# Optimization experiments

Measured on AMD Instinct MI355X. Metric: run time of the kernel, lower is better.

Reference implementation:

```python
import jax, jax.numpy as jnp
import numpy as np

B, L_SEQ, D, P, N_LAYERS, V = 2, 4096, 128, 64, 2, 32000
EPS_LN = 1e-5
EPS_Z = 1e-8


def _layernorm(x, g, b):
    mu = jnp.mean(x, axis=-1, keepdims=True)
    var = jnp.mean(jnp.square(x - mu), axis=-1, keepdims=True)
    return (x - mu) * jax.lax.rsqrt(var + EPS_LN) * g + b


def setup_inputs() -> dict:
    key = jax.random.key(0)
    ks = jax.random.split(key, 16)
    tokens = jax.random.randint(ks[0], (B, L_SEQ), 0, V)
    s = 0.02
    embed = jax.random.normal(ks[1], (V, D), jnp.float32) * s
    pos_emb = jax.random.normal(ks[2], (L_SEQ, D), jnp.float32) * s
    Wq = jax.random.normal(ks[3], (N_LAYERS, D, D), jnp.float32) * s
    Wk = jax.random.normal(ks[4], (N_LAYERS, D, D), jnp.float32) * s
    Wv = jax.random.normal(ks[5], (N_LAYERS, D, D), jnp.float32) * s
    # orthonormal random projection per layer (QR, like torch.linalg.qr reduced)
    rng = np.random.default_rng(0)
    proj_np = np.stack([np.linalg.qr(rng.standard_normal((D, P)))[0] for _ in range(N_LAYERS)])
    proj = jnp.asarray(proj_np, jnp.float32)
    ln_g = jnp.ones((N_LAYERS, D), jnp.float32)
    ln_b = jnp.zeros((N_LAYERS, D), jnp.float32)
    W1 = jax.random.normal(ks[6], (N_LAYERS, D, 4 * D), jnp.float32) * s
    b1 = jnp.zeros((N_LAYERS, 4 * D), jnp.float32)
    W2 = jax.random.normal(ks[7], (N_LAYERS, 4 * D, D), jnp.float32) * s
    b2 = jnp.zeros((N_LAYERS, D), jnp.float32)
    Wout = jax.random.normal(ks[8], (D, V), jnp.float32) * s
    return {"tokens": tokens, "embed": embed, "pos_emb": pos_emb, "Wq": Wq, "Wk": Wk,
            "Wv": Wv, "proj": proj, "ln_g": ln_g, "ln_b": ln_b, "W1": W1, "b1": b1,
            "W2": W2, "b2": b2, "Wout": Wout}


def reference(tokens, embed, pos_emb, Wq, Wk, Wv, proj, ln_g, ln_b, W1, b1, W2, b2, Wout):
    # h: [B, L, D]
    h = embed[tokens] + pos_emb[None, :, :]
    for i in range(N_LAYERS):
        residual = h
        # linear (FAVOR-style) attention, single head
        q = h @ Wq[i]
        k = h @ Wk[i]
        v = h @ Wv[i]
        q_prime = jax.nn.elu(q @ proj[i]) + 1.0  # [B, L, P]
        k_prime = jax.nn.elu(k @ proj[i]) + 1.0
        kv = jnp.einsum('blp,bld->bpd', k_prime, v)      # [B, P, D]
        num = jnp.einsum('blp,bpd->bld', q_prime, kv)     # [B, L, D]
        z = 1.0 / (jnp.sum(q_prime, axis=-1, keepdims=True) + EPS_Z)
        attn = num * z
        # LayerNorm then FFN (dropout = identity, eval mode)
        a = _layernorm(attn, ln_g[i], ln_b[i])
        f = jax.nn.gelu(a @ W1[i] + b1[i], approximate=False) @ W2[i] + b2[i]
        h = residual + f
    logits = h @ Wout  # [B, L, V]
    return logits
```

## Files before the change

kernel.cpp:

```cpp
#include <hip/hip_runtime.h>
#include <hip/hip_bf16.h>

#define BATCH 2
#define LSEQ 4096
#define M (BATCH*LSEQ)
#define D 128
#define P 64
#define NL 2
#define VOCAB 32000
#define DFF 512

typedef __attribute__((ext_vector_type(8))) short bf16x8_t;
typedef __attribute__((ext_vector_type(4))) float f32x4_t;

__device__ inline unsigned short f2bf(float f) {
    unsigned int u = __float_as_uint(f);
    unsigned int r = (u + 0x7fffu + ((u >> 16) & 1u)) >> 16;
    return (unsigned short)r;
}
__device__ inline float bf2f(unsigned short u) {
    return __uint_as_float(((unsigned int)u) << 16);
}

__global__ __launch_bounds__(256) void k_prep_all(const int* __restrict__ tokens,
                                                  const float* __restrict__ embed,
                                                  const float* __restrict__ pos,
                                                  float* __restrict__ h,
                                                  unsigned short* __restrict__ hb,
                                                  const float* __restrict__ Wout,
                                                  unsigned short* __restrict__ WT,
                                                  const float* __restrict__ Wq,
                                                  const float* __restrict__ Wk,
                                                  const float* __restrict__ Wv,
                                                  const float* __restrict__ proj,
                                                  unsigned short* __restrict__ bqkv,
                                                  const float* __restrict__ W1,
                                                  unsigned short* __restrict__ W1T,
                                                  const float* __restrict__ W2,
                                                  unsigned short* __restrict__ W2T) {
    __shared__ float tile[32][33];
    int b = blockIdx.x;
    int tid = threadIdx.x;
    if (b < 1024) {
        int gid = b * 256 + tid;
        int row = gid >> 5;
        int d4  = gid & 31;
        int l = row & (LSEQ - 1);
        int tok = tokens[row];
        float4 a = ((const float4*)(embed + (size_t)tok * D))[d4];
        float4 p4 = ((const float4*)(pos + (size_t)l * D))[d4];
        a.x += p4.x; a.y += p4.y; a.z += p4.z; a.w += p4.w;
        ((float4*)(h + (size_t)row * D))[d4] = a;
        ushort4 u; u.x = f2bf(a.x); u.y = f2bf(a.y); u.z = f2bf(a.z); u.w = f2bf(a.w);
        ((ushort4*)(hb + (size_t)row * D))[d4] = u;
    } else if (b < 5024) {
        int bb = b - 1024;
        int v0 = (bb % 1000) * 32, d0 = (bb / 1000) * 32;
        int tx = tid & 31, ty = tid >> 5;
        for (int i = ty; i < 32; i += 8)
            tile[i][tx] = Wout[(size_t)(d0 + i) * VOCAB + v0 + tx];
        __syncthreads();
        for (int i = ty; i < 32; i += 8)
            WT[(size_t)(v0 + i) * D + d0 + tx] = f2bf(tile[tx][i]);
    } else if (b < 5280) {
        int idx = (b - 5024) * 256 + tid;
        int d = idx & 127;
        int r = (idx >> 7) & 255;
        int l = idx >> 15;
        const float* WqL = Wq + (size_t)l * D * D;
        const float* WkL = Wk + (size_t)l * D * D;
        const float* WvL = Wv + (size_t)l * D * D;
        const float* pjL = proj + (size_t)l * D * P;
        float val;
        if (r < 128) {
            const float* W = (r < 64) ? WqL : WkL;
            int p = r & 63;
            float s = 0.f;
            for (int e = 0; e < D; e++) s = fmaf(W[d * D + e], pjL[e * P + p], s);
            val = s;
        } else {
            val = WvL[d * D + (r - 128)];
        }
        bqkv[((size_t)l * 256 + r) * D + d] = f2bf(val);
    } else if (b < 5792) {
        int idx = (b - 5280) * 256 + tid;
        int d = idx & 127;
        int n = (idx >> 7) & 511;
        int l = idx >> 16;
        W1T[((size_t)l * DFF + n) * D + d] = f2bf(W1[((size_t)l * D + d) * DFF + n]);
    } else {
        int idx = (b - 5792) * 256 + tid;
        int f = idx & 511;
        int n = (idx >> 9) & 127;
        int l = idx >> 16;
        W2T[((size_t)l * D + n) * DFF + f] = f2bf(W2[((size_t)l * DFF + f) * D + n]);
    }
}

__global__ __launch_bounds__(256) void k_qkvp(const unsigned short* __restrict__ hb,
                                              const unsigned short* __restrict__ Bt,
                                              float* __restrict__ qp, float* __restrict__ kp,
                                              unsigned short* __restrict__ vb,
                                              float* __restrict__ kv) {
    if (blockIdx.x == 0) {
        float4 z = make_float4(0.f, 0.f, 0.f, 0.f);
        float4* kv4 = (float4*)kv;
        for (int i = threadIdx.x; i < BATCH * P * D / 4; i += 256) kv4[i] = z;
    }
    int r0 = blockIdx.x * 32;
    int wid = threadIdx.x >> 6;
    int lane = threadIdx.x & 63;
    int c0 = wid * 64;
    int lr = lane & 15;
    int lk = (lane >> 4) * 8;
    const short* Ap = (const short*)hb;
    const short* Bp = (const short*)Bt;
    f32x4_t acc[2][4] = {};
    #pragma unroll
    for (int kc = 0; kc < 4; kc++) {
        bf16x8_t af[2], bfr[4];
        #pragma unroll
        for (int mi = 0; mi < 2; mi++)
            af[mi] = *(const bf16x8_t*)(Ap + (size_t)(r0 + mi * 16 + lr) * D + kc * 32 + lk);
        #pragma unroll
        for (int ni = 0; ni < 4; ni++)
            bfr[ni] = *(const bf16x8_t*)(Bp + (size_t)(c0 + ni * 16 + lr) * D + kc * 32 + lk);
        #pragma unroll
        for (int mi = 0; mi < 2; mi++)
            #pragma unroll
            for (int ni = 0; ni < 4; ni++)
                acc[mi][ni] = __builtin_amdgcn_mfma_f32_16x16x32_bf16(af[mi], bfr[ni], acc[mi][ni], 0, 0, 0);
    }
    int orow = (lane >> 4) * 4;
    if (wid < 2) {
        float* out = (wid == 0) ? qp : kp;
        #pragma unroll
        for (int mi = 0; mi < 2; mi++)
            #pragma unroll
            for (int ni = 0; ni < 4; ni++)
                #pragma unroll
                for (int j = 0; j < 4; j++) {
                    float x = acc[mi][ni][j];
                    float e = x > 0.f ? x + 1.f : __expf(x);
                    out[(size_t)(r0 + mi * 16 + orow + j) * P + ni * 16 + lr] = e;
                }
    } else {
        int cb = (wid - 2) * 64;
        #pragma unroll
        for (int mi = 0; mi < 2; mi++)
            #pragma unroll
            for (int ni = 0; ni < 4; ni++)
                #pragma unroll
                for (int j = 0; j < 4; j++)
                    vb[(size_t)(r0 + mi * 16 + orow + j) * D + cb + ni * 16 + lr] = f2bf(acc[mi][ni][j]);
    }
}

__global__ void k_kvpart(const float* __restrict__ kp, const unsigned short* __restrict__ vb,
                         float* __restrict__ kv) {
    int p = blockIdx.x, ch = blockIdx.y, b = blockIdx.z, d = threadIdx.x;
    const float* kpb = kp + (size_t)b * LSEQ * P + p;
    const unsigned short* vbp = vb + (size_t)b * LSEQ * D + d;
    int l0 = ch * 256;
    float a0 = 0.f, a1 = 0.f, a2 = 0.f, a3 = 0.f;
    for (int l = l0; l < l0 + 256; l += 4) {
        a0 = fmaf(kpb[(size_t)l * P],       bf2f(vbp[(size_t)l * D]),       a0);
        a1 = fmaf(kpb[(size_t)(l + 1) * P], bf2f(vbp[(size_t)(l + 1) * D]), a1);
        a2 = fmaf(kpb[(size_t)(l + 2) * P], bf2f(vbp[(size_t)(l + 2) * D]), a2);
        a3 = fmaf(kpb[(size_t)(l + 3) * P], bf2f(vbp[(size_t)(l + 3) * D]), a3);
    }
    atomicAdd(&kv[((size_t)b * P + p) * D + d], (a0 + a1) + (a2 + a3));
}

#define TSTRIDE 520
#define ABSTRIDE 136
__global__ __launch_bounds__(256) void k_attnffn(const float* __restrict__ qp,
                                                 const float* __restrict__ kv,
                                                 const float* __restrict__ lng,
                                                 const float* __restrict__ lnb,
                                                 const unsigned short* __restrict__ W1T,
                                                 const float* __restrict__ b1,
                                                 const unsigned short* __restrict__ W2T,
                                                 const float* __restrict__ b2,
                                                 float* __restrict__ h,
                                                 unsigned short* __restrict__ hb) {
    __shared__ unsigned short abt[16 * ABSTRIDE];
    __shared__ unsigned short tl[16 * TSTRIDE];
    int r0 = blockIdx.x * 16;
    int b = r0 >> 12;
    int tid = threadIdx.x;
    {
        int row16 = tid >> 4;
        int dq = tid & 15;
        int d0 = dq * 8;
        const float* qpr = qp + (size_t)(r0 + row16) * P;
        const float4* kv4 = (const float4*)(kv + (size_t)b * P * D);
        float num[8] = {};
        float zs = 0.f;
        #pragma unroll 8
        for (int p = 0; p < P; p++) {
            float qv = qpr[p];
            zs += qv;
            float4 v0 = kv4[p * 32 + dq * 2];
            float4 v1 = kv4[p * 32 + dq * 2 + 1];
            num[0] = fmaf(qv, v0.x, num[0]);
            num[1] = fmaf(qv, v0.y, num[1]);
            num[2] = fmaf(qv, v0.z, num[2]);
            num[3] = fmaf(qv, v0.w, num[3]);
            num[4] = fmaf(qv, v1.x, num[4]);
            num[5] = fmaf(qv, v1.y, num[5]);
            num[6] = fmaf(qv, v1.z, num[6]);
            num[7] = fmaf(qv, v1.w, num[7]);
        }
        float rz = 1.f / (zs + 1e-8f);
        float attn[8];
        float s = 0.f;
        #pragma unroll
        for (int j = 0; j < 8; j++) { attn[j] = num[j] * rz; s += attn[j]; }
        #pragma unroll
        for (int m = 1; m < 16; m <<= 1) s += __shfl_xor(s, m);
        float mu = s * (1.f / 128.f);
        float dv[8];
        float s2 = 0.f;
        #pragma unroll
        for (int j = 0; j < 8; j++) { dv[j] = attn[j] - mu; s2 = fmaf(dv[j], dv[j], s2); }
        #pragma unroll
        for (int m = 1; m < 16; m <<= 1) s2 += __shfl_xor(s2, m);
        float rs = rsqrtf(s2 * (1.f / 128.f) + 1e-5f);
        #pragma unroll
        for (int j = 0; j < 8; j++) {
            float o = dv[j] * rs * lng[d0 + j] + lnb[d0 + j];
            abt[row16 * ABSTRIDE + d0 + j] = f2bf(o);
        }
    }
    __syncthreads();
    int wid = tid >> 6;
    int lane = tid & 63;
    int lr = lane & 15;
    int lk = (lane >> 4) * 8;
    int orow = (lane >> 4) * 4;
    const short* B1 = (const short*)W1T;
    int c0 = wid * 128;
    f32x4_t acc1[8] = {};
    #pragma unroll
    for (int kc = 0; kc < 4; kc++) {
        bf16x8_t af = *(const bf16x8_t*)(abt + lr * ABSTRIDE + kc * 32 + lk);
        bf16x8_t bfr[8];
        #pragma unroll
        for (int ni = 0; ni < 8; ni++)
            bfr[ni] = *(const bf16x8_t*)(B1 + (size_t)(c0 + ni * 16 + lr) * D + kc * 32 + lk);
        #pragma unroll
        for (int ni = 0; ni < 8; ni++)
            acc1[ni] = __builtin_amdgcn_mfma_f32_16x16x32_bf16(af, bfr[ni], acc1[ni], 0, 0, 0);
    }
    #pragma unroll
    for (int ni = 0; ni < 8; ni++) {
        int col = c0 + ni * 16 + lr;
        float bias = b1[col];
        #pragma unroll
        for (int j = 0; j < 4; j++) {
            float x = acc1[ni][j] + bias;
            float g = 0.5f * x * (1.f + erff(x * 0.70710678f));
            tl[(orow + j) * TSTRIDE + col] = f2bf(g);
        }
    }
    __syncthreads();
    int c2 = wid * 32;
    const short* B2 = (const short*)W2T;
    f32x4_t acc2[2] = {};
    #pragma unroll 4
    for (int kc = 0; kc < 16; kc++) {
        bf16x8_t af, bfr[2];
        af = *(const bf16x8_t*)(tl + (size_t)lr * TSTRIDE + kc * 32 + lk);
        #pragma unroll
        for (int ni = 0; ni < 2; ni++)
            bfr[ni] = *(const bf16x8_t*)(B2 + (size_t)(c2 + ni * 16 + lr) * DFF + kc * 32 + lk);
        #pragma unroll
        for (int ni = 0; ni < 2; ni++)
            acc2[ni] = __builtin_amdgcn_mfma_f32_16x16x32_bf16(af, bfr[ni], acc2[ni], 0, 0, 0);
    }
    #pragma unroll
    for (int ni = 0; ni < 2; ni++) {
        int col = c2 + ni * 16 + lr;
        float bias = b2[col];
        #pragma unroll
        for (int j = 0; j < 4; j++) {
            size_t idx = (size_t)(r0 + orow + j) * D + col;
            float hn = h[idx] + acc2[ni][j] + bias;
            h[idx] = hn;
            hb[idx] = f2bf(hn);
        }
    }
}

__global__ __launch_bounds__(256) void k_gemm_out(const unsigned short* __restrict__ A,
                                                  const unsigned short* __restrict__ Bt,
                                                  float* __restrict__ C) {
    __shared__ unsigned short bl[128 * 128];
    __shared__ float cl[4][8 * 132];
    int bx = blockIdx.x;
    int bg = blockIdx.y;
    int tid = threadIdx.x;
    {
        const bf16x8_t* src = (const bf16x8_t*)((const short*)Bt + (size_t)bx * 128 * D);
        int row = tid >> 1;
        int base = (tid & 1) * 128;
        char* dst = (char*)bl + row * 256;
        #pragma unroll
        for (int i = 0; i < 8; i++) {
            int boff = base + i * 16;
            *(bf16x8_t*)(dst + (boff ^ ((row & 7) << 4))) = src[tid * 8 + i];
        }
    }
    __syncthreads();
    int wid = tid >> 6;
    int lane = tid & 63;
    int lr = lane & 15;
    int hi = lane >> 4;
    int lk = hi * 8;
    float* clw = cl[wid];
    const short* Ap = (const short*)A;
    #pragma unroll 1
    for (int w = 0; w < 4; w++) {
        int row0 = (bg * 4 + w) * 128 + wid * 32;
        f32x4_t acc[2][8] = {};
        #pragma unroll
        for (int kc = 0; kc < 4; kc++) {
            bf16x8_t af[2], bfr[8];
            #pragma unroll
            for (int mi = 0; mi < 2; mi++)
                af[mi] = *(const bf16x8_t*)(Ap + (size_t)(row0 + mi * 16 + lr) * D + kc * 32 + lk);
            #pragma unroll
            for (int ni = 0; ni < 8; ni++) {
                int brow = ni * 16 + lr;
                int boff = kc * 64 + hi * 16;
                bfr[ni] = *(const bf16x8_t*)((const char*)bl + brow * 256 + (boff ^ ((brow & 7) << 4)));
            }
            #pragma unroll
            for (int mi = 0; mi < 2; mi++)
                #pragma unroll
                for (int ni = 0; ni < 8; ni++)
                    acc[mi][ni] = __builtin_amdgcn_mfma_f32_16x16x32_bf16(af[mi], bfr[ni], acc[mi][ni], 0, 0, 0);
        }
        #pragma unroll
        for (int c = 0; c < 4; c++) {
            int mi = c >> 1;
            int hp = c & 1;
            if ((hi >> 1) == hp) {
                int rbase = (hi & 1) * 4;
                #pragma unroll
                for (int ni = 0; ni < 8; ni++)
                    #pragma unroll
                    for (int j = 0; j < 4; j++)
                        clw[(rbase + j) * 132 + ni * 16 + lr] = acc[mi][ni][j];
            }
            asm volatile("s_waitcnt lgkmcnt(0)" ::: "memory");
            float* Cb = C + (size_t)(row0 + mi * 16 + hp * 8) * VOCAB + bx * 128;
            #pragma unroll
            for (int k = 0; k < 4; k++) {
                int idx = k * 64 + lane;
                int rr = idx >> 5;
                int c4 = idx & 31;
                f32x4_t v = *(const f32x4_t*)(clw + rr * 132 + c4 * 4);
                __builtin_nontemporal_store(v, (f32x4_t*)(Cb + (size_t)rr * VOCAB + c4 * 4));
            }
            asm volatile("" ::: "memory");
        }
    }
}

extern "C" void kernel_launch(void* const* d_in, const int* in_sizes, int n_in,
                              void* d_out, int out_size, void* d_ws, size_t ws_size,
                              hipStream_t stream) {
    const int*   tokens = (const int*)d_in[0];
    const float* embed  = (const float*)d_in[1];
    const float* pos    = (const float*)d_in[2];
    const float* Wq     = (const float*)d_in[3];
    const float* Wk     = (const float*)d_in[4];
    const float* Wv     = (const float*)d_in[5];
    const float* proj   = (const float*)d_in[6];
    const float* lng    = (const float*)d_in[7];
    const float* lnb    = (const float*)d_in[8];
    const float* W1     = (const float*)d_in[9];
    const float* b1     = (const float*)d_in[10];
    const float* W2     = (const float*)d_in[11];
    const float* b2     = (const float*)d_in[12];
    const float* Wout   = (const float*)d_in[13];
    float* out = (float*)d_out;
    char* ws = (char*)d_ws;

    float*          h    = (float*)(ws);
    unsigned short* hb   = (unsigned short*)(ws + ((size_t)4  << 20));
    float*          qp   = (float*)(ws + ((size_t)6  << 20));
    float*          kp   = (float*)(ws + ((size_t)8  << 20));
    unsigned short* vb   = (unsigned short*)(ws + ((size_t)10 << 20));
    float*          kv   = (float*)(ws + ((size_t)13 << 20));
    unsigned short* wt   = (unsigned short*)(ws + ((size_t)24 << 20));
    unsigned short* bqkv = (unsigned short*)(ws + ((size_t)32 << 20));
    unsigned short* w1t  = (unsigned short*)(ws + ((size_t)33 << 20));
    unsigned short* w2t  = (unsigned short*)(ws + ((size_t)34 << 20));

    k_prep_all<<<dim3(6304), dim3(256), 0, stream>>>(tokens, embed, pos, h, hb,
                                                     Wout, wt, Wq, Wk, Wv, proj, bqkv,
                                                     W1, w1t, W2, w2t);

    for (int i = 0; i < NL; i++) {
        k_qkvp<<<dim3(M / 32), dim3(256), 0, stream>>>(hb, bqkv + (size_t)i * 256 * D, qp, kp, vb, kv);
        k_kvpart<<<dim3(P, 16, BATCH), dim3(128), 0, stream>>>(kp, vb, kv);
        k_attnffn<<<dim3(M / 16), dim3(256), 0, stream>>>(qp, kv, lng + (size_t)i * D, lnb + (size_t)i * D,
                                                          w1t + (size_t)i * DFF * D, b1 + (size_t)i * DFF,
                                                          w2t + (size_t)i * D * DFF, b2 + (size_t)i * D, h, hb);
    }

    k_gemm_out<<<dim3(VOCAB / 128, M / 128 / 4), dim3(256), 0, stream>>>(hb, wt, out);
}
```

Measured before the change: 329.3 us.

## Fuse k'ᵀv reduction into QKV projection kernel via shared memory and atomics

The separate k_kvpart kernel is removed. Each QKV block now keeps its k' and v tiles in shared memory, computes a partial k'ᵀv product, and atomically adds it into kv. The zeroing of both layers' kv buffers moves into the prep kernel. This drops one launch per layer and the global round trip of kp and vb. In exchange it issues many more contended fp32 atomics and adds shared memory and register pressure.

```diff
diff --git a/kernel.cpp b/kernel.cpp
--- a/kernel.cpp
+++ b/kernel.cpp
@@ -37,7 +37,8 @@
                                                   const float* __restrict__ W1,
                                                   unsigned short* __restrict__ W1T,
                                                   const float* __restrict__ W2,
-                                                  unsigned short* __restrict__ W2T) {
+                                                  unsigned short* __restrict__ W2T,
+                                                  float* __restrict__ kvbuf) {
     __shared__ float tile[32][33];
     int b = blockIdx.x;
     int tid = threadIdx.x;
@@ -88,28 +89,30 @@
         int n = (idx >> 7) & 511;
         int l = idx >> 16;
         W1T[((size_t)l * DFF + n) * D + d] = f2bf(W1[((size_t)l * D + d) * DFF + n]);
-    } else {
+    } else if (b < 6304) {
         int idx = (b - 5792) * 256 + tid;
         int f = idx & 511;
         int n = (idx >> 9) & 127;
         int l = idx >> 16;
         W2T[((size_t)l * D + n) * DFF + f] = f2bf(W2[((size_t)l * DFF + f) * D + n]);
+    } else {
+        float4 z = make_float4(0.f, 0.f, 0.f, 0.f);
+        float4* kv4 = (float4*)kvbuf;
+        for (int i = tid; i < NL * BATCH * P * D / 4; i += 256) kv4[i] = z;
     }
 }
 
 __global__ __launch_bounds__(256) void k_qkvp(const unsigned short* __restrict__ hb,
                                               const unsigned short* __restrict__ Bt,
-                                              float* __restrict__ qp, float* __restrict__ kp,
-                                              unsigned short* __restrict__ vb,
+                                              float* __restrict__ qp,
                                               float* __restrict__ kv) {
-    if (blockIdx.x == 0) {
-        float4 z = make_float4(0.f, 0.f, 0.f, 0.f);
-        float4* kv4 = (float4*)kv;
-        for (int i = threadIdx.x; i < BATCH * P * D / 4; i += 256) kv4[i] = z;
-    }
+    __shared__ float kpl[32 * 68];
+    __shared__ float vbl[32 * 132];
     int r0 = blockIdx.x * 32;
-    int wid = threadIdx.x >> 6;
-    int lane = threadIdx.x & 63;
+    int bb = r0 >> 12;
+    int tid = threadIdx.x;
+    int wid = tid >> 6;
+    int lane = tid & 63;
     int c0 = wid * 64;
     int lr = lane & 15;
     int lk = (lane >> 4) * 8;
@@ -132,8 +135,7 @@
                 acc[mi][ni] = __builtin_amdgcn_mfma_f32_16x16x32_bf16(af[mi], bfr[ni], acc[mi][ni], 0, 0, 0);
     }
     int orow = (lane >> 4) * 4;
-    if (wid < 2) {
-        float* out = (wid == 0) ? qp : kp;
+    if (wid == 0) {
         #pragma unroll
         for (int mi = 0; mi < 2; mi++)
             #pragma unroll
@@ -142,7 +144,18 @@
                 for (int j = 0; j < 4; j++) {
                     float x = acc[mi][ni][j];
                     float e = x > 0.f ? x + 1.f : __expf(x);
-                    out[(size_t)(r0 + mi * 16 + orow + j) * P + ni * 16 + lr] = e;
+                    qp[(size_t)(r0 + mi * 16 + orow + j) * P + ni * 16 + lr] = e;
+                }
+    } else if (wid == 1) {
+        #pragma unroll
+        for (int mi = 0; mi < 2; mi++)
+            #pragma unroll
+            for (int ni = 0; ni < 4; ni++)
+                #pragma unroll
+                for (int j = 0; j < 4; j++) {
+                    float x = acc[mi][ni][j];
+                    float e = x > 0.f ? x + 1.f : __expf(x);
+                    kpl[(mi * 16 + orow + j) * 68 + ni * 16 + lr] = e;
                 }
     } else {
         int cb = (wid - 2) * 64;
@@ -152,24 +165,27 @@
             for (int ni = 0; ni < 4; ni++)
                 #pragma unroll
                 for (int j = 0; j < 4; j++)
-                    vb[(size_t)(r0 + mi * 16 + orow + j) * D + cb + ni * 16 + lr] = f2bf(acc[mi][ni][j]);
-    }
-}
-
-__global__ void k_kvpart(const float* __restrict__ kp, const unsigned short* __restrict__ vb,
-                         float* __restrict__ kv) {
-    int p = blockIdx.x, ch = blockIdx.y, b = blockIdx.z, d = threadIdx.x;
-    const float* kpb = kp + (size_t)b * LSEQ * P + p;
-    const unsigned short* vbp = vb + (size_t)b * LSEQ * D + d;
-    int l0 = ch * 256;
-    float a0 = 0.f, a1 = 0.f, a2 = 0.f, a3 = 0.f;
-    for (int l = l0; l < l0 + 256; l += 4) {
-        a0 = fmaf(kpb[(size_t)l * P],       bf2f(vbp[(size_t)l * D]),       a0);
-        a1 = fmaf(kpb[(size_t)(l + 1) * P], bf2f(vbp[(size_t)(l + 1) * D]), a1);
-        a2 = fmaf(kpb[(size_t)(l + 2) * P], bf2f(vbp[(size_t)(l + 2) * D]), a2);
-        a3 = fmaf(kpb[(size_t)(l + 3) * P], bf2f(vbp[(size_t)(l + 3) * D]), a3);
-    }
-    atomicAdd(&kv[((size_t)b * P + p) * D + d], (a0 + a1) + (a2 + a3));
+                    vbl[(mi * 16 + orow + j) * 132 + cb + ni * 16 + lr] = bf2f(f2bf(acc[mi][ni][j]));
+    }
+    __syncthreads();
+    int p = tid & 63;
+    int dg = tid >> 6;
+    float av[32] = {};
+    for (int l = 0; l < 32; l++) {
+        float kpv = kpl[l * 68 + p];
+        #pragma unroll
+        for (int q = 0; q < 8; q++) {
+            f32x4_t v4 = *(const f32x4_t*)(vbl + l * 132 + dg * 32 + q * 4);
+            av[q * 4 + 0] = fmaf(kpv, v4[0], av[q * 4 + 0]);
+            av[q * 4 + 1] = fmaf(kpv, v4[1], av[q * 4 + 1]);
+            av[q * 4 + 2] = fmaf(kpv, v4[2], av[q * 4 + 2]);
+            av[q * 4 + 3] = fmaf(kpv, v4[3], av[q * 4 + 3]);
+        }
+    }
+    float* kvb = kv + (size_t)bb * P * D + (size_t)p * D + dg * 32;
+    #pragma unroll
+    for (int dd = 0; dd < 32; dd++)
+        atomicAdd(&kvb[dd], av[dd]);
 }
 
 #define TSTRIDE 520
@@ -392,21 +408,19 @@
     float*          h    = (float*)(ws);
     unsigned short* hb   = (unsigned short*)(ws + ((size_t)4  << 20));
     float*          qp   = (float*)(ws + ((size_t)6  << 20));
-    float*          kp   = (float*)(ws + ((size_t)8  << 20));
-    unsigned short* vb   = (unsigned short*)(ws + ((size_t)10 << 20));
-    float*          kv   = (float*)(ws + ((size_t)13 << 20));
+    float*          kvbuf= (float*)(ws + ((size_t)13 << 20));
     unsigned short* wt   = (unsigned short*)(ws + ((size_t)24 << 20));
     unsigned short* bqkv = (unsigned short*)(ws + ((size_t)32 << 20));
     unsigned short* w1t  = (unsigned short*)(ws + ((size_t)33 << 20));
     unsigned short* w2t  = (unsigned short*)(ws + ((size_t)34 << 20));
 
-    k_prep_all<<<dim3(6304), dim3(256), 0, stream>>>(tokens, embed, pos, h, hb,
+    k_prep_all<<<dim3(6305), dim3(256), 0, stream>>>(tokens, embed, pos, h, hb,
                                                      Wout, wt, Wq, Wk, Wv, proj, bqkv,
-                                                     W1, w1t, W2, w2t);
+                                                     W1, w1t, W2, w2t, kvbuf);
 
     for (int i = 0; i < NL; i++) {
-        k_qkvp<<<dim3(M / 32), dim3(256), 0, stream>>>(hb, bqkv + (size_t)i * 256 * D, qp, kp, vb, kv);
-        k_kvpart<<<dim3(P, 16, BATCH), dim3(128), 0, stream>>>(kp, vb, kv);
+        float* kv = kvbuf + (size_t)i * BATCH * P * D;
+        k_qkvp<<<dim3(M / 32), dim3(256), 0, stream>>>(hb, bqkv + (size_t)i * 256 * D, qp, kv);
         k_attnffn<<<dim3(M / 16), dim3(256), 0, stream>>>(qp, kv, lng + (size_t)i * D, lnb + (size_t)i * D,
                                                           w1t + (size_t)i * DFF * D, b1 + (size_t)i * DFF,
                                                           w2t + (size_t)i * D * DFF, b2 + (size_t)i * D, h, hb);
```

Result: slower. 504.5 us (+53.2%).
